# Optimization experiments

Measured on AMD Instinct MI355X. Metric: run time of the kernel, lower is better.

## Reference

```python
import jax, jax.numpy as jnp
import numpy as np

VOCAB = 16000
DIM = 1024
B, T = 4, 2048


def setup_inputs() -> dict:
    key = jax.random.key(0)
    k_ids, k_emb, k_w, k_lw, k_lb = jax.random.split(key, 5)
    input_ids = jax.random.randint(k_ids, (B, T), 0, VOCAB)
    embed = jax.random.normal(k_emb, (VOCAB, DIM), dtype=jnp.float32)
    # w_state = I + 0.05 * (default Linear init ~ U(-1/sqrt(dim), 1/sqrt(dim)))
    bound = 1.0 / np.sqrt(DIM)
    w_state = jnp.eye(DIM, dtype=jnp.float32) + 0.05 * jax.random.uniform(
        k_w, (DIM, DIM), minval=-bound, maxval=bound, dtype=jnp.float32)
    lm_w = jax.random.uniform(k_lw, (VOCAB, DIM), minval=-bound, maxval=bound, dtype=jnp.float32)
    lm_b = jax.random.uniform(k_lb, (VOCAB,), minval=-bound, maxval=bound, dtype=jnp.float32)
    return {"input_ids": input_ids, "embed": embed, "w_state": w_state,
            "lm_w": lm_w, "lm_b": lm_b}


def reference(input_ids, embed, w_state, lm_w, lm_b):
    # h: [B, T, D]
    h = embed[input_ids]
    state0 = jnp.zeros((h.shape[0], h.shape[2]), dtype=h.dtype)

    def step(state, h_t):
        # nn.Linear: state @ W^T ; then add input injection
        new_state = state @ w_state.T + h_t
        return new_state, new_state

    # scan over time: inputs [T, B, D]
    _, outs = jax.lax.scan(step, state0, jnp.swapaxes(h, 0, 1))
    hidden = jnp.swapaxes(outs, 0, 1)  # [B, T, D]
    logits = hidden @ lm_w.T + lm_b    # [B, T, V]
    return logits
```

## Files before the change

### kernel.cpp

```cpp
#include <hip/hip_runtime.h>
#include <hip/hip_bf16.h>
#include <stdint.h>

#define DD 1024
#define BB 4
#define TT 2048
#define VV 16000
#define LCH 8
#define NR 1024
#define PADR 512
#define NPAD 16128

typedef __bf16 bf16_t;
typedef float f32x4_t __attribute__((ext_vector_type(4)));
typedef bf16_t bf16x8_t __attribute__((ext_vector_type(8)));
typedef bf16_t bf16x4_t __attribute__((ext_vector_type(4)));

#define MODE_PLAIN 0
#define MODE_ROUND 1
#define MODE_LEVEL 2
#define MODE_CARRY 3

#define KIND_SQ 0
#define KIND_ROUND 1
#define KIND_LEVEL 2
#define KIND_CARRY 3

struct Job {
  const float* A; const float* B; float* C; const float* Cin;
  int kind; int dlt;
};
struct Jobs { Job j[8]; };

__global__ __launch_bounds__(256) void k_cvt(const float* __restrict__ src,
                                             bf16_t* __restrict__ dst, int n4) {
  int i = blockIdx.x * blockDim.x + threadIdx.x;
  int stride = gridDim.x * blockDim.x;
  for (; i < n4; i += stride) {
    float4 v = ((const float4*)src)[i];
    union { ushort4 u; bf16_t h[4]; } p;
    p.h[0] = (bf16_t)v.x; p.h[1] = (bf16_t)v.y;
    p.h[2] = (bf16_t)v.z; p.h[3] = (bf16_t)v.w;
    ((ushort4*)dst)[i] = p.u;
  }
}

__global__ __launch_bounds__(256) void k_gather(const float* __restrict__ embed,
                                                const int* __restrict__ ids,
                                                float* __restrict__ slab0) {
  int r = blockIdx.x;
  int b = r & 3, c = r >> 2;
  int id = ids[b * TT + c * LCH];
  const float4* s = (const float4*)(embed + (size_t)id * DD);
  float4* d = (float4*)(slab0 + (size_t)r * DD);
  for (int i = threadIdx.x; i < DD / 4; i += blockDim.x) d[i] = s[i];
}

template <int NS>
__device__ __forceinline__ void swrite(char* base, int byteoff, float4 v) {
  float r0 = v.x, r1 = v.y, r2 = v.z, r3 = v.w;
#pragma unroll
  for (int p = 0; p < NS; ++p) {
    bf16x4_t h;
    h[0] = (bf16_t)r0; h[1] = (bf16_t)r1; h[2] = (bf16_t)r2; h[3] = (bf16_t)r3;
    *(bf16x4_t*)(base + p * 5120 + byteoff) = h;
    if (p + 1 < NS) {
      r0 -= (float)h[0]; r1 -= (float)h[1]; r2 -= (float)h[2]; r3 -= (float)h[3];
    }
  }
}

template <int NS, bool NN, int MODE>
__device__ __forceinline__ void mbody(bf16_t* __restrict__ SB, const Job& jb,
                                      const float* __restrict__ embed,
                                      const int* __restrict__ ids,
                                      bf16_t* __restrict__ hidden) {
  const float* A = jb.A;
  const float* Bm = jb.B;
  const int tid = threadIdx.x, lane = tid & 63, wave = tid >> 6;
  const int i0 = blockIdx.y * 64, j0 = blockIdx.x * 64;
  const int wm = (wave >> 1) * 32, wn = (wave & 1) * 32;
  char* Ap = (char*)SB;
  char* Bp = Ap + NS * 5120;
  const int arow = tid >> 2;
  const int akb = (tid & 3) * 8;
  const int bj = tid & 63, bk4 = (tid >> 6) * 4;
  const int frow = lane & 15, fkb = (lane >> 4) * 16;
  f32x4_t acc[2][2] = {};

  const float* Aptr = A + (size_t)(i0 + arow) * DD + (tid & 3) * 4;
  const float* BptrNT = Bm + (size_t)(j0 + arow) * DD + (tid & 3) * 4;
  const float* BptrNN = Bm + (size_t)bk4 * DD + j0 + bj;

  float4 a0 = *(const float4*)(Aptr);
  float4 a1 = *(const float4*)(Aptr + 16);
  float4 b0, b1;
  float s0[4], s1[4];
  if (!NN) {
    b0 = *(const float4*)(BptrNT);
    b1 = *(const float4*)(BptrNT + 16);
  } else {
#pragma unroll
    for (int s = 0; s < 4; ++s) s0[s] = BptrNN[(size_t)s * DD];
#pragma unroll
    for (int s = 0; s < 4; ++s) s1[s] = BptrNN[(size_t)(16 + s) * DD];
  }

  for (int k0 = 0;;) {
    __syncthreads();
    swrite<NS>(Ap, arow * 80 + akb, a0);
    swrite<NS>(Ap, arow * 80 + akb + 32, a1);
    if (!NN) {
      swrite<NS>(Bp, arow * 80 + akb, b0);
      swrite<NS>(Bp, arow * 80 + akb + 32, b1);
    } else {
      float4 t0; t0.x = s0[0]; t0.y = s0[1]; t0.z = s0[2]; t0.w = s0[3];
      float4 t1; t1.x = s1[0]; t1.y = s1[1]; t1.z = s1[2]; t1.w = s1[3];
      swrite<NS>(Bp, bj * 80 + bk4 * 2, t0);
      swrite<NS>(Bp, bj * 80 + bk4 * 2 + 32, t1);
    }
    __syncthreads();
    int kn = k0 + 32;
    if (kn < DD) {
      a0 = *(const float4*)(Aptr + kn);
      a1 = *(const float4*)(Aptr + kn + 16);
      if (!NN) {
        b0 = *(const float4*)(BptrNT + kn);
        b1 = *(const float4*)(BptrNT + kn + 16);
      } else {
#pragma unroll
        for (int s = 0; s < 4; ++s) s0[s] = BptrNN[(size_t)(kn + s) * DD];
#pragma unroll
        for (int s = 0; s < 4; ++s) s1[s] = BptrNN[(size_t)(kn + 16 + s) * DD];
      }
    }
    bf16x8_t af[NS][2], bfx[NS][2];
#pragma unroll
    for (int p = 0; p < NS; ++p)
#pragma unroll
      for (int mf = 0; mf < 2; ++mf) {
        af[p][mf] = *(const bf16x8_t*)(Ap + p * 5120 + (wm + mf * 16 + frow) * 80 + fkb);
        bfx[p][mf] = *(const bf16x8_t*)(Bp + p * 5120 + (wn + mf * 16 + frow) * 80 + fkb);
      }
#pragma unroll
    for (int pa = 0; pa < NS; ++pa)
#pragma unroll
      for (int pb = 0; pb < NS; ++pb) {
        if (pa + pb < NS) {
#pragma unroll
          for (int mf = 0; mf < 2; ++mf)
#pragma unroll
            for (int nf = 0; nf < 2; ++nf)
              acc[mf][nf] = __builtin_amdgcn_mfma_f32_16x16x32_bf16(
                  af[pa][mf], bfx[pb][nf], acc[mf][nf], 0, 0, 0);
        }
      }
    k0 = kn;
    if (k0 >= DD) break;
  }

  const int ecol = lane & 15, er4 = (lane >> 4) * 4;
#pragma unroll
  for (int mf = 0; mf < 2; ++mf) {
#pragma unroll
    for (int nf = 0; nf < 2; ++nf) {
      const int rb = i0 + wm + mf * 16 + er4;
      const int cj = j0 + wn + nf * 16 + ecol;
#pragma unroll
      for (int rg = 0; rg < 4; ++rg) {
        const int ri = rb + rg;
        float v = acc[mf][nf][rg];
        if (MODE == MODE_PLAIN) {
          jb.C[(size_t)ri * DD + cj] = v;
        } else if (MODE == MODE_ROUND) {
          int b = ri & 3, c = ri >> 2, t = c * LCH + jb.dlt;
          v += embed[(size_t)ids[b * TT + t] * DD + cj];
          jb.C[(size_t)ri * DD + cj] = v;
        } else if (MODE == MODE_LEVEL) {
          v += jb.Cin[(size_t)ri * DD + cj];
          jb.C[(size_t)ri * DD + cj] = v;
        } else {
          int b = ri & 3, c = ri >> 2, t = c * LCH + jb.dlt;
          hidden[((size_t)b * TT + t) * DD + cj] =
              (bf16_t)(v + jb.Cin[(size_t)ri * DD + cj]);
        }
      }
    }
  }
}

__global__ __launch_bounds__(256, 2) void k_multi(Jobs jobs,
                                                  const float* __restrict__ embed,
                                                  const int* __restrict__ ids,
                                                  bf16_t* __restrict__ hidden) {
  __shared__ __align__(16) bf16_t SB[6 * 2560];
  const Job& jb = jobs.j[blockIdx.z];
  if (jb.kind == KIND_SQ)
    mbody<3, true, MODE_PLAIN>(SB, jb, embed, ids, hidden);
  else if (jb.kind == KIND_ROUND)
    mbody<2, false, MODE_ROUND>(SB, jb, embed, ids, hidden);
  else if (jb.kind == KIND_LEVEL)
    mbody<2, false, MODE_LEVEL>(SB, jb, embed, ids, hidden);
  else
    mbody<2, false, MODE_CARRY>(SB, jb, embed, ids, hidden);
}

__device__ __forceinline__ void gload16(const void* g, void* l) {
  __builtin_amdgcn_global_load_lds((const __attribute__((address_space(1))) void*)g,
                                   (__attribute__((address_space(3))) void*)l, 16, 0, 0);
}

#define NTK 32

__global__ __launch_bounds__(512, 2) void k_lmhead2(
    const bf16_t* __restrict__ Ah, const bf16_t* __restrict__ Bw,
    const float* __restrict__ bias, float* __restrict__ Cout) {
  __shared__ __align__(16) char LB[4 * 32768];
  const int tid = threadIdx.x, lane = tid & 63, wave = tid >> 6;
  const int wr = wave >> 2, wc = wave & 3;
  int orig = blockIdx.y * gridDim.x + blockIdx.x;
  int swz = (orig & 7) * 252 + (orig >> 3);
  int by = swz / 63, bx = swz % 63;
  const int m0 = by * 256, n0 = bx * 256;

  const int srow = tid >> 2;
  const int scb = (tid & 3) * 16;

  auto stage = [&](int t) {
    char* buf = LB + (size_t)(t & 3) * 32768;
#pragma unroll
    for (int p = 0; p < 2; ++p) {
      int row = p * 128 + srow;
      int sw = ((row >> 1) & 3) << 4;
      gload16((const char*)Ah + ((size_t)(m0 + row) * DD + t * 32) * 2 + (scb ^ sw),
              buf + p * 8192 + wave * 1024);
      gload16((const char*)Bw + ((size_t)(n0 + row) * DD + t * 32) * 2 + (scb ^ sw),
              buf + 16384 + p * 8192 + wave * 1024);
    }
  };

  const int frow = lane & 15;
  const int c4b = (lane >> 4) * 16;
  f32x4_t acc[8][4] = {};

  stage(0); stage(1); stage(2);
  asm volatile("s_waitcnt vmcnt(8)\ns_barrier" ::: "memory");

  for (int t = 0; t < NTK; ++t) {
    char* Abuf = LB + (size_t)(t & 3) * 32768;
    char* Bbuf = Abuf + 16384;
    if (t + 3 < NTK) stage(t + 3);
    bf16x8_t afr[4], bfr[4];
#pragma unroll
    for (int nf = 0; nf < 4; ++nf) {
      int r = wc * 64 + nf * 16 + frow;
      bfr[nf] = *(const bf16x8_t*)(Bbuf + r * 64 + (c4b ^ (((r >> 1) & 3) << 4)));
    }
#pragma unroll
    for (int mf = 0; mf < 4; ++mf) {
      int r = wr * 128 + mf * 16 + frow;
      afr[mf] = *(const bf16x8_t*)(Abuf + r * 64 + (c4b ^ (((r >> 1) & 3) << 4)));
    }
    __builtin_amdgcn_s_setprio(1);
#pragma unroll
    for (int mf = 0; mf < 4; ++mf)
#pragma unroll
      for (int nf = 0; nf < 4; ++nf)
        acc[mf][nf] = __builtin_amdgcn_mfma_f32_16x16x32_bf16(
            afr[mf], bfr[nf], acc[mf][nf], 0, 0, 0);
    __builtin_amdgcn_s_setprio(0);
#pragma unroll
    for (int mf = 0; mf < 4; ++mf) {
      int r = wr * 128 + 64 + mf * 16 + frow;
      afr[mf] = *(const bf16x8_t*)(Abuf + r * 64 + (c4b ^ (((r >> 1) & 3) << 4)));
    }
    __builtin_amdgcn_s_setprio(1);
#pragma unroll
    for (int mf = 0; mf < 4; ++mf)
#pragma unroll
      for (int nf = 0; nf < 4; ++nf)
        acc[4 + mf][nf] = __builtin_amdgcn_mfma_f32_16x16x32_bf16(
            afr[mf], bfr[nf], acc[4 + mf][nf], 0, 0, 0);
    __builtin_amdgcn_s_setprio(0);
    if (t < NTK - 3) {
      asm volatile("s_waitcnt vmcnt(8)\ns_barrier" ::: "memory");
    } else if (t == NTK - 3) {
      asm volatile("s_waitcnt vmcnt(4)\ns_barrier" ::: "memory");
    } else if (t == NTK - 2) {
      asm volatile("s_waitcnt vmcnt(0)\ns_barrier" ::: "memory");
    }
  }

  const int ecol = lane & 15, er4 = (lane >> 4) * 4;
#pragma unroll
  for (int mf = 0; mf < 8; ++mf) {
#pragma unroll
    for (int nf = 0; nf < 4; ++nf) {
      int gm = m0 + wr * 128 + mf * 16 + er4;
      int gn = n0 + wc * 64 + nf * 16 + ecol;
      if (gn < VV) {
        float bv = bias[gn];
#pragma unroll
        for (int rg = 0; rg < 4; ++rg)
          Cout[(size_t)(gm + rg) * VV + gn] = acc[mf][nf][rg] + bv;
      }
    }
  }
}

extern "C" void kernel_launch(void* const* d_in, const int* in_sizes, int n_in,
                              void* d_out, int out_size, void* d_ws, size_t ws_size,
                              hipStream_t stream) {
  (void)in_sizes; (void)n_in; (void)out_size; (void)ws_size;
  const int* ids = (const int*)d_in[0];
  const float* embed = (const float*)d_in[1];
  const float* w_state = (const float*)d_in[2];
  const float* lm_w = (const float*)d_in[3];
  const float* lm_b = (const float*)d_in[4];
  float* out = (float*)d_out;

  const size_t M1 = (size_t)DD * DD;
  float* PW = (float*)d_ws;
  float* Q = PW + 8 * M1;
  float* LOC = Q + 7 * M1;
  float* E0 = LOC + 8 * M1;
  float* E1 = E0 + (size_t)(PADR + NR) * DD;
  bf16_t* HID = (bf16_t*)(E1 + (size_t)(PADR + NR) * DD);
  bf16_t* LWB = HID + (size_t)BB * TT * DD;
  float* E0d = E0 + (size_t)PADR * DD;
  float* E1d = E1 + (size_t)PADR * DD;

  k_cvt<<<2048, 256, 0, stream>>>(lm_w, LWB, VV * DD / 4);
  hipMemsetAsync(LWB + (size_t)VV * DD, 0,
                 (size_t)(NPAD - VV) * DD * sizeof(bf16_t), stream);
  hipMemcpyAsync(PW, w_state, M1 * sizeof(float), hipMemcpyDeviceToDevice, stream);
  k_gather<<<NR, 256, 0, stream>>>(embed, ids, LOC);
  hipMemsetAsync(E0, 0, (size_t)PADR * DD * sizeof(float), stream);
  hipMemsetAsync(E1, 0, (size_t)PADR * DD * sizeof(float), stream);

  Jobs J{};
  J.j[0] = Job{w_state, w_state, PW + M1, nullptr, KIND_SQ, 0};
  J.j[1] = Job{LOC, w_state, LOC + M1, nullptr, KIND_ROUND, 1};
  k_multi<<<dim3(16, 16, 2), 256, 0, stream>>>(J, embed, ids, HID);
  J.j[0] = Job{PW + M1, w_state, PW + 2 * M1, nullptr, KIND_SQ, 0};
  J.j[1] = Job{PW + M1, PW + M1, PW + 3 * M1, nullptr, KIND_SQ, 0};
  J.j[2] = Job{LOC + M1, w_state, LOC + 2 * M1, nullptr, KIND_ROUND, 2};
  k_multi<<<dim3(16, 16, 3), 256, 0, stream>>>(J, embed, ids, HID);
  J.j[0] = Job{PW + 3 * M1, w_state, PW + 4 * M1, nullptr, KIND_SQ, 0};
  J.j[1] = Job{PW + 3 * M1, PW + M1, PW + 5 * M1, nullptr, KIND_SQ, 0};
  J.j[2] = Job{PW + 3 * M1, PW + 2 * M1, PW + 6 * M1, nullptr, KIND_SQ, 0};
  J.j[3] = Job{PW + 3 * M1, PW + 3 * M1, PW + 7 * M1, nullptr, KIND_SQ, 0};
  J.j[4] = Job{LOC + 2 * M1, w_state, LOC + 3 * M1, nullptr, KIND_ROUND, 3};
  k_multi<<<dim3(16, 16, 5), 256, 0, stream>>>(J, embed, ids, HID);
  for (int d = 4; d <= 7; ++d) {
    const float* src = (d == 4) ? (PW + 7 * M1) : (Q + (size_t)(d - 5) * M1);
    J.j[0] = Job{src, src, Q + (size_t)(d - 4) * M1, nullptr, KIND_SQ, 0};
    J.j[1] = Job{LOC + (size_t)(d - 1) * M1, w_state, LOC + (size_t)d * M1,
                 nullptr, KIND_ROUND, d};
    k_multi<<<dim3(16, 16, 2), 256, 0, stream>>>(J, embed, ids, HID);
  }
  hipMemcpyAsync(E0d, LOC + 7 * M1, M1 * sizeof(float),
                 hipMemcpyDeviceToDevice, stream);

  float* inp = E0d;
  float* outp = E1d;
  for (int k = 0; k < 8; ++k) {
    Jobs J2{};
    int nz = 0;
    if (k <= 2) {
      const float* src = Q + (size_t)(k + 3) * M1;
      J2.j[nz++] = Job{src, src, Q + (size_t)(k + 4) * M1, nullptr, KIND_SQ, 0};
    }
    const float* Bq = (k == 0) ? (PW + 7 * M1) : (Q + (size_t)(k - 1) * M1);
    J2.j[nz++] = Job{inp - (size_t)(4 << k) * DD, Bq, outp, inp, KIND_LEVEL, 0};
    k_multi<<<dim3(16, 16, nz), 256, 0, stream>>>(J2, embed, ids, HID);
    float* t = inp; inp = outp; outp = t;
  }

  Jobs Jc{};
  for (int d = 0; d < 8; ++d)
    Jc.j[d] = Job{inp - (size_t)4 * DD, PW + (size_t)d * M1, nullptr,
                  LOC + (size_t)d * M1, KIND_CARRY, d};
  k_multi<<<dim3(16, 16, 8), 256, 0, stream>>>(Jc, embed, ids, HID);

  dim3 gl(NPAD / 256, (BB * TT) / 256);
  k_lmhead2<<<gl, 512, 0, stream>>>(HID, LWB, lm_b, out);
}
```

Before: 900.1 us.

## Store scan state as split bf16 pairs and drop LDS staging for state GEMMs

The chunked-scan state slabs (LOC, E0/E1) are now kept as hi/lo bf16 pairs instead of fp32, so state GEMMs load pre-split A fragments straight from global memory into MFMA registers without LDS staging or barriers. Row shifting for the level passes is done by index offset with zero-fill for negative rows, which replaces the padded zero regions and their memsets. The B operand is split into hi/lo on the fly from fp32, and only three of the four cross terms are computed. This halves state memory traffic and removes syncs, but it loses LDS reuse of operands across waves and may cost some precision.

New measurement: 1.132 ms. 25.8% more time.

```diff
diff --git a/kernel.cpp b/kernel.cpp
--- a/kernel.cpp
+++ b/kernel.cpp
@@ -8,29 +8,23 @@
 #define VV 16000
 #define LCH 8
 #define NR 1024
-#define PADR 512
 #define NPAD 16128
+#define M1C ((size_t)DD * DD)
 
 typedef __bf16 bf16_t;
 typedef float f32x4_t __attribute__((ext_vector_type(4)));
 typedef bf16_t bf16x8_t __attribute__((ext_vector_type(8)));
 typedef bf16_t bf16x4_t __attribute__((ext_vector_type(4)));
 
-#define MODE_PLAIN 0
-#define MODE_ROUND 1
-#define MODE_LEVEL 2
-#define MODE_CARRY 3
-
 #define KIND_SQ 0
 #define KIND_ROUND 1
 #define KIND_LEVEL 2
 #define KIND_CARRY 3
 
-struct Job {
-  const float* A; const float* B; float* C; const float* Cin;
-  int kind; int dlt;
-};
-struct Jobs { Job j[8]; };
+__device__ __forceinline__ void gload16(const void* g, void* l) {
+  __builtin_amdgcn_global_load_lds((const __attribute__((address_space(1))) void*)g,
+                                   (__attribute__((address_space(3))) void*)l, 16, 0, 0);
+}
 
 __global__ __launch_bounds__(256) void k_cvt(const float* __restrict__ src,
                                              bf16_t* __restrict__ dst, int n4) {
@@ -45,16 +39,32 @@
   }
 }
 
-__global__ __launch_bounds__(256) void k_gather(const float* __restrict__ embed,
-                                                const int* __restrict__ ids,
-                                                float* __restrict__ slab0) {
+__global__ __launch_bounds__(256) void k_gather2(const float* __restrict__ embed,
+                                                 const int* __restrict__ ids,
+                                                 bf16_t* __restrict__ slab0) {
   int r = blockIdx.x;
   int b = r & 3, c = r >> 2;
   int id = ids[b * TT + c * LCH];
   const float4* s = (const float4*)(embed + (size_t)id * DD);
-  float4* d = (float4*)(slab0 + (size_t)r * DD);
-  for (int i = threadIdx.x; i < DD / 4; i += blockDim.x) d[i] = s[i];
-}
+  bf16_t* p0 = slab0 + (size_t)r * DD;
+  bf16_t* p1 = p0 + M1C;
+  for (int i = threadIdx.x; i < DD / 4; i += blockDim.x) {
+    float4 v = s[i];
+    union { ushort4 u; bf16_t h[4]; } a, bq;
+    a.h[0] = (bf16_t)v.x; bq.h[0] = (bf16_t)(v.x - (float)a.h[0]);
+    a.h[1] = (bf16_t)v.y; bq.h[1] = (bf16_t)(v.y - (float)a.h[1]);
+    a.h[2] = (bf16_t)v.z; bq.h[2] = (bf16_t)(v.z - (float)a.h[2]);
+    a.h[3] = (bf16_t)v.w; bq.h[3] = (bf16_t)(v.w - (float)a.h[3]);
+    ((ushort4*)p0)[i] = a.u;
+    ((ushort4*)p1)[i] = bq.u;
+  }
+}
+
+struct JobC {
+  const void* A; const void* B; void* C; const void* Cin;
+  int kind; int dlt; int shift;
+};
+struct JobsC { JobC j[8]; };
 
 template <int NS>
 __device__ __forceinline__ void swrite(char* base, int byteoff, float4 v) {
@@ -70,18 +80,15 @@
   }
 }
 
-template <int NS, bool NN, int MODE>
-__device__ __forceinline__ void mbody(bf16_t* __restrict__ SB, const Job& jb,
-                                      const float* __restrict__ embed,
-                                      const int* __restrict__ ids,
-                                      bf16_t* __restrict__ hidden) {
-  const float* A = jb.A;
-  const float* Bm = jb.B;
+__device__ __forceinline__ void mbodySQ(bf16_t* __restrict__ SBb, const JobC& jb) {
+  const float* A = (const float*)jb.A;
+  const float* Bm = (const float*)jb.B;
+  float* Cm = (float*)jb.C;
   const int tid = threadIdx.x, lane = tid & 63, wave = tid >> 6;
   const int i0 = blockIdx.y * 64, j0 = blockIdx.x * 64;
   const int wm = (wave >> 1) * 32, wn = (wave & 1) * 32;
-  char* Ap = (char*)SB;
-  char* Bp = Ap + NS * 5120;
+  char* Ap = (char*)SBb;
+  char* Bp = Ap + 3 * 5120;
   const int arow = tid >> 2;
   const int akb = (tid & 3) * 8;
   const int bj = tid & 63, bk4 = (tid >> 6) * 4;
@@ -89,64 +96,47 @@
   f32x4_t acc[2][2] = {};
 
   const float* Aptr = A + (size_t)(i0 + arow) * DD + (tid & 3) * 4;
-  const float* BptrNT = Bm + (size_t)(j0 + arow) * DD + (tid & 3) * 4;
   const float* BptrNN = Bm + (size_t)bk4 * DD + j0 + bj;
 
   float4 a0 = *(const float4*)(Aptr);
   float4 a1 = *(const float4*)(Aptr + 16);
-  float4 b0, b1;
   float s0[4], s1[4];
-  if (!NN) {
-    b0 = *(const float4*)(BptrNT);
-    b1 = *(const float4*)(BptrNT + 16);
-  } else {
-#pragma unroll
-    for (int s = 0; s < 4; ++s) s0[s] = BptrNN[(size_t)s * DD];
-#pragma unroll
-    for (int s = 0; s < 4; ++s) s1[s] = BptrNN[(size_t)(16 + s) * DD];
-  }
+#pragma unroll
+  for (int s = 0; s < 4; ++s) s0[s] = BptrNN[(size_t)s * DD];
+#pragma unroll
+  for (int s = 0; s < 4; ++s) s1[s] = BptrNN[(size_t)(16 + s) * DD];
 
   for (int k0 = 0;;) {
     __syncthreads();
-    swrite<NS>(Ap, arow * 80 + akb, a0);
-    swrite<NS>(Ap, arow * 80 + akb + 32, a1);
-    if (!NN) {
-      swrite<NS>(Bp, arow * 80 + akb, b0);
-      swrite<NS>(Bp, arow * 80 + akb + 32, b1);
-    } else {
-      float4 t0; t0.x = s0[0]; t0.y = s0[1]; t0.z = s0[2]; t0.w = s0[3];
-      float4 t1; t1.x = s1[0]; t1.y = s1[1]; t1.z = s1[2]; t1.w = s1[3];
-      swrite<NS>(Bp, bj * 80 + bk4 * 2, t0);
-      swrite<NS>(Bp, bj * 80 + bk4 * 2 + 32, t1);
-    }
+    swrite<3>(Ap, arow * 80 + akb, a0);
+    swrite<3>(Ap, arow * 80 + akb + 32, a1);
+    float4 t0; t0.x = s0[0]; t0.y = s0[1]; t0.z = s0[2]; t0.w = s0[3];
+    float4 t1; t1.x = s1[0]; t1.y = s1[1]; t1.z = s1[2]; t1.w = s1[3];
+    swrite<3>(Bp, bj * 80 + bk4 * 2, t0);
+    swrite<3>(Bp, bj * 80 + bk4 * 2 + 32, t1);
     __syncthreads();
     int kn = k0 + 32;
     if (kn < DD) {
       a0 = *(const float4*)(Aptr + kn);
       a1 = *(const float4*)(Aptr + kn + 16);
-      if (!NN) {
-        b0 = *(const float4*)(BptrNT + kn);
-        b1 = *(const float4*)(BptrNT + kn + 16);
-      } else {
-#pragma unroll
-        for (int s = 0; s < 4; ++s) s0[s] = BptrNN[(size_t)(kn + s) * DD];
-#pragma unroll
-        for (int s = 0; s < 4; ++s) s1[s] = BptrNN[(size_t)(kn + 16 + s) * DD];
-      }
-    }
-    bf16x8_t af[NS][2], bfx[NS][2];
-#pragma unroll
-    for (int p = 0; p < NS; ++p)
+#pragma unroll
+      for (int s = 0; s < 4; ++s) s0[s] = BptrNN[(size_t)(kn + s) * DD];
+#pragma unroll
+      for (int s = 0; s < 4; ++s) s1[s] = BptrNN[(size_t)(kn + 16 + s) * DD];
+    }
+    bf16x8_t af[3][2], bfx[3][2];
+#pragma unroll
+    for (int p = 0; p < 3; ++p)
 #pragma unroll
       for (int mf = 0; mf < 2; ++mf) {
         af[p][mf] = *(const bf16x8_t*)(Ap + p * 5120 + (wm + mf * 16 + frow) * 80 + fkb);
         bfx[p][mf] = *(const bf16x8_t*)(Bp + p * 5120 + (wn + mf * 16 + frow) * 80 + fkb);
       }
 #pragma unroll
-    for (int pa = 0; pa < NS; ++pa)
-#pragma unroll
-      for (int pb = 0; pb < NS; ++pb) {
-        if (pa + pb < NS) {
+    for (int pa = 0; pa < 3; ++pa)
+#pragma unroll
+      for (int pb = 0; pb < 3; ++pb) {
+        if (pa + pb < 3) {
 #pragma unroll
           for (int mf = 0; mf < 2; ++mf)
 #pragma unroll
@@ -161,53 +151,115 @@
 
   const int ecol = lane & 15, er4 = (lane >> 4) * 4;
 #pragma unroll
-  for (int mf = 0; mf < 2; ++mf) {
+  for (int mf = 0; mf < 2; ++mf)
+#pragma unroll
+    for (int nf = 0; nf < 2; ++nf)
+#pragma unroll
+      for (int rg = 0; rg < 4; ++rg)
+        Cm[(size_t)(i0 + wm + mf * 16 + er4 + rg) * DD + (j0 + wn + nf * 16 + ecol)] =
+            acc[mf][nf][rg];
+}
+
+template <int MODE>
+__device__ __forceinline__ void sbody(const JobC& jb,
+                                      const float* __restrict__ embed,
+                                      const int* __restrict__ ids,
+                                      bf16_t* __restrict__ hid) {
+  const bf16_t* Ab = (const bf16_t*)jb.A;
+  const float* Bf = (const float*)jb.B;
+  const int tid = threadIdx.x, lane = tid & 63, wave = tid >> 6;
+  const int i0 = blockIdx.y * 64, j0 = blockIdx.x * 64;
+  const int wm = (wave >> 1) * 32, wn = (wave & 1) * 32;
+  const int frow = lane & 15, fq = lane >> 4;
+  const int shift = jb.shift;
+  const int ar0 = i0 + wm + frow - shift;
+  const int rb0 = j0 + wn + frow;
+  f32x4_t acc[2][2] = {};
+
+  for (int k0 = 0; k0 < DD; k0 += 32) {
+    const int kk = k0 + fq * 8;
+    bf16x8_t a0[2], a1[2];
+#pragma unroll
+    for (int mf = 0; mf < 2; ++mf) {
+      int r = ar0 + mf * 16;
+      if (r >= 0) {
+        const bf16_t* ap = Ab + (size_t)r * DD + kk;
+        a0[mf] = *(const bf16x8_t*)ap;
+        a1[mf] = *(const bf16x8_t*)(ap + M1C);
+      } else {
+        a0[mf] = bf16x8_t{};
+        a1[mf] = bf16x8_t{};
+      }
+    }
+    bf16x8_t b0[2], b1[2];
 #pragma unroll
     for (int nf = 0; nf < 2; ++nf) {
-      const int rb = i0 + wm + mf * 16 + er4;
-      const int cj = j0 + wn + nf * 16 + ecol;
+      const float* bp = Bf + (size_t)(rb0 + nf * 16) * DD + kk;
+      float4 x = *(const float4*)bp;
+      float4 y = *(const float4*)(bp + 4);
+      float xs[8] = {x.x, x.y, x.z, x.w, y.x, y.y, y.z, y.w};
+#pragma unroll
+      for (int e = 0; e < 8; ++e) {
+        bf16_t h = (bf16_t)xs[e];
+        b0[nf][e] = h;
+        b1[nf][e] = (bf16_t)(xs[e] - (float)h);
+      }
+    }
+#pragma unroll
+    for (int mf = 0; mf < 2; ++mf)
+#pragma unroll
+      for (int nf = 0; nf < 2; ++nf) {
+        acc[mf][nf] = __builtin_amdgcn_mfma_f32_16x16x32_bf16(
+            a0[mf], b0[nf], acc[mf][nf], 0, 0, 0);
+        acc[mf][nf] = __builtin_amdgcn_mfma_f32_16x16x32_bf16(
+            a0[mf], b1[nf], acc[mf][nf], 0, 0, 0);
+        acc[mf][nf] = __builtin_amdgcn_mfma_f32_16x16x32_bf16(
+            a1[mf], b0[nf], acc[mf][nf], 0, 0, 0);
+      }
+  }
+
+  const int ecol = lane & 15;
+#pragma unroll
+  for (int mf = 0; mf < 2; ++mf)
+#pragma unroll
+    for (int nf = 0; nf < 2; ++nf)
 #pragma unroll
       for (int rg = 0; rg < 4; ++rg) {
-        const int ri = rb + rg;
+        int ri = i0 + wm + mf * 16 + fq * 4 + rg;
+        int cj = j0 + wn + nf * 16 + ecol;
         float v = acc[mf][nf][rg];
-        if (MODE == MODE_PLAIN) {
-          jb.C[(size_t)ri * DD + cj] = v;
-        } else if (MODE == MODE_ROUND) {
+        size_t o = (size_t)ri * DD + cj;
+        if (MODE == 1) {
           int b = ri & 3, c = ri >> 2, t = c * LCH + jb.dlt;
           v += embed[(size_t)ids[b * TT + t] * DD + cj];
-          jb.C[(size_t)ri * DD + cj] = v;
-        } else if (MODE == MODE_LEVEL) {
-          v += jb.Cin[(size_t)ri * DD + cj];
-          jb.C[(size_t)ri * DD + cj] = v;
+          bf16_t* Co = (bf16_t*)jb.C;
+          bf16_t h0 = (bf16_t)v;
+          Co[o] = h0; Co[o + M1C] = (bf16_t)(v - (float)h0);
+        } else if (MODE == 2) {
+          const bf16_t* Ci = (const bf16_t*)jb.Cin;
+          v += (float)Ci[o] + (float)Ci[o + M1C];
+          bf16_t* Co = (bf16_t*)jb.C;
+          bf16_t h0 = (bf16_t)v;
+          Co[o] = h0; Co[o + M1C] = (bf16_t)(v - (float)h0);
         } else {
+          const bf16_t* Ci = (const bf16_t*)jb.Cin;
+          v += (float)Ci[o] + (float)Ci[o + M1C];
           int b = ri & 3, c = ri >> 2, t = c * LCH + jb.dlt;
-          hidden[((size_t)b * TT + t) * DD + cj] =
-              (bf16_t)(v + jb.Cin[(size_t)ri * DD + cj]);
+          hid[((size_t)b * TT + t) * DD + cj] = (bf16_t)v;
         }
       }
-    }
-  }
-}
-
-__global__ __launch_bounds__(256, 2) void k_multi(Jobs jobs,
+}
+
+__global__ __launch_bounds__(256, 2) void k_chain(JobsC jobs,
                                                   const float* __restrict__ embed,
                                                   const int* __restrict__ ids,
-                                                  bf16_t* __restrict__ hidden) {
-  __shared__ __align__(16) bf16_t SB[6 * 2560];
-  const Job& jb = jobs.j[blockIdx.z];
-  if (jb.kind == KIND_SQ)
-    mbody<3, true, MODE_PLAIN>(SB, jb, embed, ids, hidden);
-  else if (jb.kind == KIND_ROUND)
-    mbody<2, false, MODE_ROUND>(SB, jb, embed, ids, hidden);
-  else if (jb.kind == KIND_LEVEL)
-    mbody<2, false, MODE_LEVEL>(SB, jb, embed, ids, hidden);
-  else
-    mbody<2, false, MODE_CARRY>(SB, jb, embed, ids, hidden);
-}
-
-__device__ __forceinline__ void gload16(const void* g, void* l) {
-  __builtin_amdgcn_global_load_lds((const __attribute__((address_space(1))) void*)g,
-                                   (__attribute__((address_space(3))) void*)l, 16, 0, 0);
+                                                  bf16_t* __restrict__ hid) {
+  __shared__ __align__(16) bf16_t SBb[6 * 2560];
+  const JobC& jb = jobs.j[blockIdx.z];
+  if (jb.kind == KIND_SQ) mbodySQ(SBb, jb);
+  else if (jb.kind == KIND_ROUND) sbody<1>(jb, embed, ids, hid);
+  else if (jb.kind == KIND_LEVEL) sbody<2>(jb, embed, ids, hid);
+  else sbody<3>(jb, embed, ids, hid);
 }
 
 #define NTK 32
@@ -319,69 +371,73 @@
   const float* lm_b = (const float*)d_in[4];
   float* out = (float*)d_out;
 
-  const size_t M1 = (size_t)DD * DD;
+  const size_t M1 = M1C;
   float* PW = (float*)d_ws;
-  float* Q = PW + 8 * M1;
-  float* LOC = Q + 7 * M1;
-  float* E0 = LOC + 8 * M1;
-  float* E1 = E0 + (size_t)(PADR + NR) * DD;
-  bf16_t* HID = (bf16_t*)(E1 + (size_t)(PADR + NR) * DD);
-  bf16_t* LWB = HID + (size_t)BB * TT * DD;
-  float* E0d = E0 + (size_t)PADR * DD;
-  float* E1d = E1 + (size_t)PADR * DD;
+  float* Qf = PW + 8 * M1;
+  bf16_t* LOCb = (bf16_t*)(Qf + 7 * M1);
+  bf16_t* E0 = LOCb + 16 * M1;
+  bf16_t* E1 = E0 + 2 * M1;
+  bf16_t* HID = E1 + 2 * M1;
+  bf16_t* LWB = HID + 8 * M1;
 
   k_cvt<<<2048, 256, 0, stream>>>(lm_w, LWB, VV * DD / 4);
   hipMemsetAsync(LWB + (size_t)VV * DD, 0,
                  (size_t)(NPAD - VV) * DD * sizeof(bf16_t), stream);
   hipMemcpyAsync(PW, w_state, M1 * sizeof(float), hipMemcpyDeviceToDevice, stream);
-  k_gather<<<NR, 256, 0, stream>>>(embed, ids, LOC);
-  hipMemsetAsync(E0, 0, (size_t)PADR * DD * sizeof(float), stream);
-  hipMemsetAsync(E1, 0, (size_t)PADR * DD * sizeof(float), stream);
-
-  Jobs J{};
-  J.j[0] = Job{w_state, w_state, PW + M1, nullptr, KIND_SQ, 0};
-  J.j[1] = Job{LOC, w_state, LOC + M1, nullptr, KIND_ROUND, 1};
-  k_multi<<<dim3(16, 16, 2), 256, 0, stream>>>(J, embed, ids, HID);
-  J.j[0] = Job{PW + M1, w_state, PW + 2 * M1, nullptr, KIND_SQ, 0};
-  J.j[1] = Job{PW + M1, PW + M1, PW + 3 * M1, nullptr, KIND_SQ, 0};
-  J.j[2] = Job{LOC + M1, w_state, LOC + 2 * M1, nullptr, KIND_ROUND, 2};
-  k_multi<<<dim3(16, 16, 3), 256, 0, stream>>>(J, embed, ids, HID);
-  J.j[0] = Job{PW + 3 * M1, w_state, PW + 4 * M1, nullptr, KIND_SQ, 0};
-  J.j[1] = Job{PW + 3 * M1, PW + M1, PW + 5 * M1, nullptr, KIND_SQ, 0};
-  J.j[2] = Job{PW + 3 * M1, PW + 2 * M1, PW + 6 * M1, nullptr, KIND_SQ, 0};
-  J.j[3] = Job{PW + 3 * M1, PW + 3 * M1, PW + 7 * M1, nullptr, KIND_SQ, 0};
-  J.j[4] = Job{LOC + 2 * M1, w_state, LOC + 3 * M1, nullptr, KIND_ROUND, 3};
-  k_multi<<<dim3(16, 16, 5), 256, 0, stream>>>(J, embed, ids, HID);
+  k_gather2<<<NR, 256, 0, stream>>>(embed, ids, LOCb);
+
+  auto SQ = [&](const float* A, const float* B, float* C) {
+    return JobC{A, B, C, nullptr, KIND_SQ, 0, 0};
+  };
+  auto RD = [&](int d) {
+    return JobC{LOCb + (size_t)(d - 1) * 2 * M1, w_state,
+                LOCb + (size_t)d * 2 * M1, nullptr, KIND_ROUND, d, 0};
+  };
+
+  JobsC J{};
+  J.j[0] = SQ(w_state, w_state, PW + M1);
+  J.j[1] = RD(1);
+  k_chain<<<dim3(16, 16, 2), 256, 0, stream>>>(J, embed, ids, HID);
+  J.j[0] = SQ(PW + M1, w_state, PW + 2 * M1);
+  J.j[1] = SQ(PW + M1, PW + M1, PW + 3 * M1);
+  J.j[2] = RD(2);
+  k_chain<<<dim3(16, 16, 3), 256, 0, stream>>>(J, embed, ids, HID);
+  J.j[0] = SQ(PW + 3 * M1, w_state, PW + 4 * M1);
+  J.j[1] = SQ(PW + 3 * M1, PW + M1, PW + 5 * M1);
+  J.j[2] = SQ(PW + 3 * M1, PW + 2 * M1, PW + 6 * M1);
+  J.j[3] = SQ(PW + 3 * M1, PW + 3 * M1, PW + 7 * M1);
+  J.j[4] = RD(3);
+  k_chain<<<dim3(16, 16, 5), 256, 0, stream>>>(J, embed, ids, HID);
   for (int d = 4; d <= 7; ++d) {
-    const float* src = (d == 4) ? (PW + 7 * M1) : (Q + (size_t)(d - 5) * M1);
-    J.j[0] = Job{src, src, Q + (size_t)(d - 4) * M1, nullptr, KIND_SQ, 0};
-    J.j[1] = Job{LOC + (size_t)(d - 1) * M1, w_state, LOC + (size_t)d * M1,
-                 nullptr, KIND_ROUND, d};
-    k_multi<<<dim3(16, 16, 2), 256, 0, stream>>>(J, embed, ids, HID);
-  }
-  hipMemcpyAsync(E0d, LOC + 7 * M1, M1 * sizeof(float),
+    int j = d - 4;
+    const float* src = (j == 0) ? (PW + 7 * M1) : (Qf + (size_t)(j - 1) * M1);
+    J.j[0] = SQ(src, src, Qf + (size_t)j * M1);
+    J.j[1] = RD(d);
+    k_chain<<<dim3(16, 16, 2), 256, 0, stream>>>(J, embed, ids, HID);
+  }
+  hipMemcpyAsync(E0, LOCb + 14 * M1, 2 * M1 * sizeof(bf16_t),
                  hipMemcpyDeviceToDevice, stream);
 
-  float* inp = E0d;
-  float* outp = E1d;
+  bf16_t* inp = E0;
+  bf16_t* outp = E1;
   for (int k = 0; k < 8; ++k) {
-    Jobs J2{};
+    JobsC J2{};
     int nz = 0;
     if (k <= 2) {
-      const float* src = Q + (size_t)(k + 3) * M1;
-      J2.j[nz++] = Job{src, src, Q + (size_t)(k + 4) * M1, nullptr, KIND_SQ, 0};
-    }
-    const float* Bq = (k == 0) ? (PW + 7 * M1) : (Q + (size_t)(k - 1) * M1);
-    J2.j[nz++] = Job{inp - (size_t)(4 << k) * DD, Bq, outp, inp, KIND_LEVEL, 0};
-    k_multi<<<dim3(16, 16, nz), 256, 0, stream>>>(J2, embed, ids, HID);
-    float* t = inp; inp = outp; outp = t;
-  }
-
-  Jobs Jc{};
+      const float* src = Qf + (size_t)(k + 3) * M1;
+      J2.j[nz++] = SQ(src, src, Qf + (size_t)(k + 4) * M1);
+    }
+    const float* Bq = (k == 0) ? (PW + 7 * M1) : (Qf + (size_t)(k - 1) * M1);
+    J2.j[nz++] = JobC{inp, Bq, outp, inp, KIND_LEVEL, 0, 4 << k};
+    k_chain<<<dim3(16, 16, nz), 256, 0, stream>>>(J2, embed, ids, HID);
+    bf16_t* t = inp; inp = outp; outp = t;
+  }
+
+  JobsC Jc{};
   for (int d = 0; d < 8; ++d)
-    Jc.j[d] = Job{inp - (size_t)4 * DD, PW + (size_t)d * M1, nullptr,
-                  LOC + (size_t)d * M1, KIND_CARRY, d};
-  k_multi<<<dim3(16, 16, 8), 256, 0, stream>>>(Jc, embed, ids, HID);
+    Jc.j[d] = JobC{inp, PW + (size_t)d * M1, nullptr,
+                   LOCb + (size_t)d * 2 * M1, KIND_CARRY, d, 4};
+  k_chain<<<dim3(16, 16, 8), 256, 0, stream>>>(Jc, embed, ids, HID);
 
   dim3 gl(NPAD / 256, (BB * TT) / 256);
   k_lmhead2<<<gl, 512, 0, stream>>>(HID, LWB, lm_b, out);
```
